# Kernel tuning notes

Measured on AMD Instinct MI355X. Metric: run time of the kernel, lower is better.

Reference implementation:

```python
import math
import jax, jax.numpy as jnp
import numpy as np

B, T, C = 4, 2048, 1024
N_HEAD = 16
HEAD_DIM = C // N_HEAD

def setup_inputs() -> dict:
    key = jax.random.key(0)
    k0, k1, k2, k3, k4 = jax.random.split(key, 5)
    s = 1.0 / math.sqrt(C)
    return {
        "x": jax.random.normal(k0, (B, T, C), dtype=jnp.float32),
        "W_q": jax.random.normal(k1, (C, C), dtype=jnp.float32) * s,
        "W_k": jax.random.normal(k2, (C, C), dtype=jnp.float32) * s,
        "W_v": jax.random.normal(k3, (C, C), dtype=jnp.float32) * s,
        "W_o": jax.random.normal(k4, (C, C), dtype=jnp.float32) * s,
    }

def reference(x, W_q, W_k, W_v, W_o):
    b, t, c = x.shape
    h, hd = N_HEAD, HEAD_DIM
    # nn.Linear(y) = y @ W.T ; project and split heads -> [B, H, T, hd]
    q = (x @ W_q.T).reshape(b, t, h, hd).transpose(0, 2, 1, 3)
    k = (x @ W_k.T).reshape(b, t, h, hd).transpose(0, 2, 1, 3)
    v = (x @ W_v.T).reshape(b, t, h, hd).transpose(0, 2, 1, 3)
    # scores [B, H, T, T], causal mask, stable softmax
    attn = jnp.einsum('bhqd,bhkd->bhqk', q, k) / math.sqrt(hd)
    causal = jnp.tril(jnp.ones((t, t), dtype=bool))
    attn = jnp.where(causal[None, None], attn, -jnp.inf)
    attn = jax.nn.softmax(attn, axis=-1)
    out = jnp.einsum('bhqk,bhkd->bhqd', attn, v)
    out = out.transpose(0, 2, 1, 3).reshape(b, t, c)
    return out @ W_o.T
```

## Files before the change

### kernel.cpp

```cpp
#include <hip/hip_runtime.h>
#include <math.h>

#define Bsz 4
#define Tsz 2048
#define Csz 1024
#define NH  16
#define HD  64

typedef short bf16x8 __attribute__((ext_vector_type(8)));
typedef float f32x4  __attribute__((ext_vector_type(4)));
typedef unsigned short u16;
typedef unsigned int uint;

typedef const __attribute__((address_space(1))) unsigned int gas_uint;
typedef __attribute__((address_space(3))) unsigned int las_uint;

__device__ __forceinline__ void async_cp16(const u16* g, u16* l) {
    __builtin_amdgcn_global_load_lds((gas_uint*)g, (las_uint*)l, 16, 0, 0);
}

__device__ __forceinline__ u16 f2bf(float f) {
    union { float f; unsigned u; } v; v.f = f;
    unsigned r = v.u + 0x7fffu + ((v.u >> 16) & 1u);
    return (u16)(r >> 16);
}

__global__ void cast_kernel(const float* __restrict__ src, u16* __restrict__ dst, int n) {
    int i = (blockIdx.x * blockDim.x + threadIdx.x) * 8;
    if (i + 8 <= n) {
        float4 a = *(const float4*)(src + i);
        float4 b = *(const float4*)(src + i + 4);
        bf16x8 o;
        o[0] = (short)f2bf(a.x); o[1] = (short)f2bf(a.y);
        o[2] = (short)f2bf(a.z); o[3] = (short)f2bf(a.w);
        o[4] = (short)f2bf(b.x); o[5] = (short)f2bf(b.y);
        o[6] = (short)f2bf(b.z); o[7] = (short)f2bf(b.w);
        *(bf16x8*)(dst + i) = o;
    } else {
        for (; i < n; i++) dst[i] = f2bf(src[i]);
    }
}

__global__ void cast3_kernel(const float* __restrict__ s0, const float* __restrict__ s1,
                             const float* __restrict__ s2, u16* __restrict__ dst) {
    const int NW = Csz * Csz;
    int i = (blockIdx.x * blockDim.x + threadIdx.x) * 8;
    int m = i >> 20;
    int local = i & (NW - 1);
    const float* src = (m == 0) ? s0 : (m == 1) ? s1 : s2;
    float4 a = *(const float4*)(src + local);
    float4 b = *(const float4*)(src + local + 4);
    bf16x8 o;
    o[0] = (short)f2bf(a.x); o[1] = (short)f2bf(a.y);
    o[2] = (short)f2bf(a.z); o[3] = (short)f2bf(a.w);
    o[4] = (short)f2bf(b.x); o[5] = (short)f2bf(b.y);
    o[6] = (short)f2bf(b.z); o[7] = (short)f2bf(b.w);
    *(bf16x8*)(dst + i) = o;
}

__global__ void gemm_qkv(const u16* __restrict__ A, const u16* __restrict__ Bm,
                         u16* __restrict__ Qo, u16* __restrict__ Ko, u16* __restrict__ Vo,
                         float qscale) {
    const int K = Csz;
    __shared__ u16 sA[128 * 32];
    __shared__ u16 sB[128 * 32];
    const int tid  = threadIdx.x;
    const int wave = tid >> 6, lane = tid & 63;
    const int lr = lane & 15, lq = lane >> 4;
    const int m0 = blockIdx.y * 128, n0 = blockIdx.x * 128;
    const int wm = (wave & 1) * 64, wn = (wave >> 1) * 64;

    const int srow = lane >> 2;
    const int scol = (lane & 3) * 8;
    const u16* gA = A  + (size_t)(m0 + wave * 32 + srow) * K + scol;
    const u16* gB = Bm + (size_t)(n0 + wave * 32 + srow) * K + scol;
    u16* lA = sA + wave * 1024;
    u16* lB = sB + wave * 1024;

    f32x4 acc[4][4] = {};

    for (int k0 = 0; k0 < K; k0 += 32) {
        __syncthreads();
        async_cp16(gA + k0,                  lA);
        async_cp16(gA + (size_t)16 * K + k0, lA + 512);
        async_cp16(gB + k0,                  lB);
        async_cp16(gB + (size_t)16 * K + k0, lB + 512);
        __syncthreads();

        bf16x8 af[4], bfv[4];
        #pragma unroll
        for (int f = 0; f < 4; f++)
            af[f]  = *(const bf16x8*)(sA + (wm + f * 16 + lr) * 32 + lq * 8);
        #pragma unroll
        for (int f = 0; f < 4; f++)
            bfv[f] = *(const bf16x8*)(sB + (wn + f * 16 + lr) * 32 + lq * 8);
        #pragma unroll
        for (int i = 0; i < 4; i++)
            #pragma unroll
            for (int j = 0; j < 4; j++)
                acc[i][j] = __builtin_amdgcn_mfma_f32_16x16x32_bf16(af[i], bfv[j], acc[i][j], 0, 0, 0);
    }

    const int sel = n0 >> 10;
    const float scale = (sel == 0) ? qscale : 1.0f;
    u16* dst = (sel == 0) ? Qo : (sel == 1) ? Ko : Vo;

    #pragma unroll
    for (int i = 0; i < 4; i++) {
        #pragma unroll
        for (int j = 0; j < 4; j++) {
            #pragma unroll
            for (int r = 0; r < 4; r++) {
                int m = m0 + wm + i * 16 + lq * 4 + r;
                int n = (n0 & 1023) + wn + j * 16 + lr;
                int b = m >> 11, t = m & (Tsz - 1);
                int h = n >> 6,  d = n & (HD - 1);
                u16 bv = f2bf(acc[i][j][r] * scale);
                if (sel == 2)
                    Vo[(((size_t)b * NH + h) * HD + d) * Tsz + t] = bv;
                else
                    dst[(((size_t)b * NH + h) * Tsz + t) * HD + d] = bv;
            }
        }
    }
}

__global__ __launch_bounds__(256, 2)
void gemm_out(const u16* __restrict__ A, const u16* __restrict__ Bm,
              float* __restrict__ out) {
    const int K = Csz, N = Csz;
    __shared__ u16 sA[128 * 32];
    __shared__ u16 sB[128 * 32];
    const int tid  = threadIdx.x;
    const int wave = tid >> 6, lane = tid & 63;
    const int lr = lane & 15, lq = lane >> 4;
    const int m0 = blockIdx.y * 128, n0 = blockIdx.x * 128;
    const int wm = (wave & 1) * 64, wn = (wave >> 1) * 64;

    const int srow = lane >> 2;
    const int scol = (lane & 3) * 8;
    const u16* gA = A  + (size_t)(m0 + wave * 32 + srow) * K + scol;
    const u16* gB = Bm + (size_t)(n0 + wave * 32 + srow) * K + scol;
    u16* lA = sA + wave * 1024;
    u16* lB = sB + wave * 1024;

    f32x4 acc[4][4] = {};

    for (int k0 = 0; k0 < K; k0 += 32) {
        __syncthreads();
        async_cp16(gA + k0,                  lA);
        async_cp16(gA + (size_t)16 * K + k0, lA + 512);
        async_cp16(gB + k0,                  lB);
        async_cp16(gB + (size_t)16 * K + k0, lB + 512);
        __syncthreads();

        bf16x8 af[4], bfv[4];
        #pragma unroll
        for (int f = 0; f < 4; f++)
            af[f]  = *(const bf16x8*)(sA + (wm + f * 16 + lr) * 32 + lq * 8);
        #pragma unroll
        for (int f = 0; f < 4; f++)
            bfv[f] = *(const bf16x8*)(sB + (wn + f * 16 + lr) * 32 + lq * 8);
        #pragma unroll
        for (int i = 0; i < 4; i++)
            #pragma unroll
            for (int j = 0; j < 4; j++)
                acc[i][j] = __builtin_amdgcn_mfma_f32_16x16x32_bf16(af[i], bfv[j], acc[i][j], 0, 0, 0);
    }

    #pragma unroll
    for (int i = 0; i < 4; i++)
        #pragma unroll
        for (int j = 0; j < 4; j++)
            #pragma unroll
            for (int r = 0; r < 4; r++) {
                int m = m0 + wm + i * 16 + lq * 4 + r;
                int n = n0 + wn + j * 16 + lr;
                out[(size_t)m * N + n] = acc[i][j][r];
            }
}

#define LDT 72

__global__ __launch_bounds__(256, 4)
void attn_kernel(const u16* __restrict__ Q, const u16* __restrict__ Kb,
                 const u16* __restrict__ Vt, u16* __restrict__ O) {
    __shared__ u16 sK[64 * LDT];
    __shared__ u16 sV[64 * LDT];
    __shared__ u16 sP[4][16 * LDT];
    const int tid  = threadIdx.x;
    const int wave = tid >> 6, lane = tid & 63;
    const int lr = lane & 15, lq = lane >> 4;
    const int bh = blockIdx.y;
    const int qa = blockIdx.x;
    const int qc = 31 - qa;
    const int ta = qa * 64, tc = qc * 64;

    const u16* Qp = Q  + (size_t)bh * Tsz * HD;
    const u16* Kp = Kb + (size_t)bh * Tsz * HD;
    const u16* Vp = Vt + (size_t)bh * HD * Tsz;

    bf16x8 qfA0 = *(const bf16x8*)(Qp + (size_t)(ta + wave * 16 + lr) * HD + lq * 8);
    bf16x8 qfA1 = *(const bf16x8*)(Qp + (size_t)(ta + wave * 16 + lr) * HD + 32 + lq * 8);
    bf16x8 qfC0 = *(const bf16x8*)(Qp + (size_t)(tc + wave * 16 + lr) * HD + lq * 8);
    bf16x8 qfC1 = *(const bf16x8*)(Qp + (size_t)(tc + wave * 16 + lr) * HD + 32 + lq * 8);

    f32x4 accOA[4] = {}, accOC[4] = {};
    f32x4 accLA = {}, accLC = {};

    bf16x8 ones;
    #pragma unroll
    for (int i = 0; i < 8; i++) ones[i] = (short)0x3F80;

#define PROCESS(T0, QF0, QF1, ACCO, ACCL, DIAG)                                       \
    {                                                                                 \
        f32x4 accS[4];                                                                \
        _Pragma("unroll")                                                             \
        for (int j = 0; j < 4; j++) {                                                 \
            bf16x8 b0 = *(const bf16x8*)(sK + (j * 16 + lr) * LDT + lq * 8);          \
            bf16x8 b1 = *(const bf16x8*)(sK + (j * 16 + lr) * LDT + 32 + lq * 8);     \
            f32x4 z = {};                                                             \
            z = __builtin_amdgcn_mfma_f32_16x16x32_bf16(QF0, b0, z, 0, 0, 0);         \
            z = __builtin_amdgcn_mfma_f32_16x16x32_bf16(QF1, b1, z, 0, 0, 0);         \
            accS[j] = z;                                                              \
        }                                                                             \
        _Pragma("unroll")                                                             \
        for (int r = 0; r < 4; r++) {                                                 \
            const int rowg = (T0) + wave * 16 + lq * 4 + r;                           \
            _Pragma("unroll")                                                         \
            for (int j = 0; j < 4; j++) {                                             \
                float v = accS[j][r];                                                 \
                if (DIAG && (kb * 64 + j * 16 + lr > rowg)) v = -200.0f;              \
                sP[wave][(lq * 4 + r) * LDT + j * 16 + lr] =                          \
                    f2bf(__builtin_amdgcn_exp2f(v));                                  \
            }                                                                         \
        }                                                                             \
        _Pragma("unroll")                                                             \
        for (int ks = 0; ks < 2; ks++) {                                              \
            bf16x8 pf = *(const bf16x8*)(&sP[wave][0] + lr * LDT + ks * 32 + lq * 8); \
            ACCL = __builtin_amdgcn_mfma_f32_16x16x32_bf16(pf, ones, ACCL, 0, 0, 0);  \
            _Pragma("unroll")                                                         \
            for (int j = 0; j < 4; j++) {                                             \
                bf16x8 vf = *(const bf16x8*)(sV + (j * 16 + lr) * LDT + ks * 32 + lq * 8); \
                ACCO[j] = __builtin_amdgcn_mfma_f32_16x16x32_bf16(pf, vf, ACCO[j], 0, 0, 0); \
            }                                                                         \
        }                                                                             \
    }

    for (int kb = 0; kb <= qc; kb++) {
        __syncthreads();
        #pragma unroll
        for (int c = tid; c < 512; c += 256) {
            int row = c >> 3, dc = (c & 7) * 8;
            *(bf16x8*)(sK + row * LDT + dc) =
                *(const bf16x8*)(Kp + (size_t)(kb * 64 + row) * HD + dc);
            *(bf16x8*)(sV + row * LDT + dc) =
                *(const bf16x8*)(Vp + (size_t)row * Tsz + kb * 64 + dc);
        }
        __syncthreads();
        if (kb <= qa) PROCESS(ta, qfA0, qfA1, accOA, accLA, (kb == qa));
        PROCESS(tc, qfC0, qfC1, accOC, accLC, (kb == qc));
    }
#undef PROCESS

    const int b = bh >> 4, h = bh & 15;
    #pragma unroll
    for (int j = 0; j < 4; j++) {
        #pragma unroll
        for (int r = 0; r < 4; r++) {
            int t = wave * 16 + lq * 4 + r;
            int d = j * 16 + lr;
            O[((size_t)b * Tsz + ta + t) * Csz + h * HD + d] = f2bf(accOA[j][r] / accLA[r]);
            O[((size_t)b * Tsz + tc + t) * Csz + h * HD + d] = f2bf(accOC[j][r] / accLC[r]);
        }
    }
}

extern "C" void kernel_launch(void* const* d_in, const int* in_sizes, int n_in,
                              void* d_out, int out_size, void* d_ws, size_t ws_size,
                              hipStream_t stream) {
    const float* x  = (const float*)d_in[0];
    const float* Wq = (const float*)d_in[1];
    const float* Wk = (const float*)d_in[2];
    const float* Wv = (const float*)d_in[3];
    const float* Wo = (const float*)d_in[4];
    float* out = (float*)d_out;

    const size_t NX = (size_t)Bsz * Tsz * Csz;
    const size_t NW = (size_t)Csz * Csz;

    char* ws = (char*)d_ws;
    u16* xb   = (u16*)ws; ws += NX * 2;
    u16* wqkv = (u16*)ws; ws += 3 * NW * 2;
    u16* wob  = (u16*)ws; ws += NW * 2;
    u16* qbuf = (u16*)ws; ws += NX * 2;
    u16* kbuf = (u16*)ws; ws += NX * 2;
    u16* vtb  = (u16*)ws; ws += NX * 2;
    u16* abuf = (u16*)ws; ws += NX * 2;

    cast_kernel<<<dim3((unsigned)(NX / 2048)), 256, 0, stream>>>(x, xb, (int)NX);
    cast3_kernel<<<dim3((unsigned)(3 * NW / 2048)), 256, 0, stream>>>(Wq, Wk, Wv, wqkv);
    cast_kernel<<<dim3((unsigned)(NW / 2048)), 256, 0, stream>>>(Wo, wob, (int)NW);

    const float qscale = 0.125f * 1.44269504088896340736f;
    gemm_qkv<<<dim3(24, 64), 256, 0, stream>>>(xb, wqkv, qbuf, kbuf, vtb, qscale);

    attn_kernel<<<dim3(16, Bsz * NH), 256, 0, stream>>>(qbuf, kbuf, vtb, abuf);

    gemm_out<<<dim3(8, 64), 256, 0, stream>>>(abuf, wob, out);
}
```

Before: 295.4 us.

## Double K-step in GEMMs, vectorize V stores, transpose QK^T to pack P writes

Both GEMM kernels now load two 32-wide K slices per barrier pair, which halves the number of __syncthreads per tile at the cost of double the LDS. The QKV epilogue writes the transposed V tile as packed 4-element bf16 stores. Attention computes S transposed (K as the A operand, Q as B) so each lane holds 4 consecutive keys, allowing packed bf16 stores into the P scratch instead of scalar 16-bit writes. It also uses a cheaper round-half-up bf16 pack, which slightly changes rounding.

```diff
diff --git a/kernel.cpp b/kernel.cpp
--- a/kernel.cpp
+++ b/kernel.cpp
@@ -23,6 +23,11 @@
     union { float f; unsigned u; } v; v.f = f;
     unsigned r = v.u + 0x7fffu + ((v.u >> 16) & 1u);
     return (u16)(r >> 16);
+}
+
+__device__ __forceinline__ uint pkbf(float a, float b) {
+    union { float f; uint u; } x, y; x.f = a; y.f = b;
+    return ((x.u + 0x8000u) >> 16) | ((y.u + 0x8000u) & 0xFFFF0000u);
 }
 
 __global__ void cast_kernel(const float* __restrict__ src, u16* __restrict__ dst, int n) {
@@ -58,12 +63,13 @@
     *(bf16x8*)(dst + i) = o;
 }
 
-__global__ void gemm_qkv(const u16* __restrict__ A, const u16* __restrict__ Bm,
-                         u16* __restrict__ Qo, u16* __restrict__ Ko, u16* __restrict__ Vo,
-                         float qscale) {
+__global__ __launch_bounds__(256, 2)
+void gemm_qkv(const u16* __restrict__ A, const u16* __restrict__ Bm,
+              u16* __restrict__ Qo, u16* __restrict__ Ko, u16* __restrict__ Vo,
+              float qscale) {
     const int K = Csz;
-    __shared__ u16 sA[128 * 32];
-    __shared__ u16 sB[128 * 32];
+    __shared__ u16 sA0[128 * 32], sA1[128 * 32];
+    __shared__ u16 sB0[128 * 32], sB1[128 * 32];
     const int tid  = threadIdx.x;
     const int wave = tid >> 6, lane = tid & 63;
     const int lr = lane & 15, lq = lane >> 4;
@@ -74,54 +80,74 @@
     const int scol = (lane & 3) * 8;
     const u16* gA = A  + (size_t)(m0 + wave * 32 + srow) * K + scol;
     const u16* gB = Bm + (size_t)(n0 + wave * 32 + srow) * K + scol;
-    u16* lA = sA + wave * 1024;
-    u16* lB = sB + wave * 1024;
+    u16* lA0 = sA0 + wave * 1024; u16* lA1 = sA1 + wave * 1024;
+    u16* lB0 = sB0 + wave * 1024; u16* lB1 = sB1 + wave * 1024;
 
     f32x4 acc[4][4] = {};
 
-    for (int k0 = 0; k0 < K; k0 += 32) {
-        __syncthreads();
-        async_cp16(gA + k0,                  lA);
-        async_cp16(gA + (size_t)16 * K + k0, lA + 512);
-        async_cp16(gB + k0,                  lB);
-        async_cp16(gB + (size_t)16 * K + k0, lB + 512);
-        __syncthreads();
-
-        bf16x8 af[4], bfv[4];
-        #pragma unroll
-        for (int f = 0; f < 4; f++)
-            af[f]  = *(const bf16x8*)(sA + (wm + f * 16 + lr) * 32 + lq * 8);
-        #pragma unroll
-        for (int f = 0; f < 4; f++)
-            bfv[f] = *(const bf16x8*)(sB + (wn + f * 16 + lr) * 32 + lq * 8);
+#define QKV_COMPUTE(SA, SB)                                                          \
+    {                                                                                \
+        bf16x8 af[4], bfv[4];                                                        \
+        _Pragma("unroll")                                                            \
+        for (int f = 0; f < 4; f++)                                                  \
+            af[f]  = *(const bf16x8*)((SA) + (wm + f * 16 + lr) * 32 + lq * 8);      \
+        _Pragma("unroll")                                                            \
+        for (int f = 0; f < 4; f++)                                                  \
+            bfv[f] = *(const bf16x8*)((SB) + (wn + f * 16 + lr) * 32 + lq * 8);      \
+        _Pragma("unroll")                                                            \
+        for (int i = 0; i < 4; i++)                                                  \
+            _Pragma("unroll")                                                        \
+            for (int j = 0; j < 4; j++)                                              \
+                acc[i][j] = __builtin_amdgcn_mfma_f32_16x16x32_bf16(af[i], bfv[j], acc[i][j], 0, 0, 0); \
+    }
+
+    for (int k0 = 0; k0 < K; k0 += 64) {
+        __syncthreads();
+        async_cp16(gA + k0,                       lA0);
+        async_cp16(gA + (size_t)16 * K + k0,      lA0 + 512);
+        async_cp16(gA + k0 + 32,                  lA1);
+        async_cp16(gA + (size_t)16 * K + k0 + 32, lA1 + 512);
+        async_cp16(gB + k0,                       lB0);
+        async_cp16(gB + (size_t)16 * K + k0,      lB0 + 512);
+        async_cp16(gB + k0 + 32,                  lB1);
+        async_cp16(gB + (size_t)16 * K + k0 + 32, lB1 + 512);
+        __syncthreads();
+        QKV_COMPUTE(sA0, sB0);
+        QKV_COMPUTE(sA1, sB1);
+    }
+#undef QKV_COMPUTE
+
+    const int sel = n0 >> 10;
+    if (sel == 2) {
+        #pragma unroll
+        for (int i = 0; i < 4; i++) {
+            #pragma unroll
+            for (int j = 0; j < 4; j++) {
+                int m = m0 + wm + i * 16 + lq * 4;
+                int b = m >> 11, t = m & (Tsz - 1);
+                int n = (n0 & 1023) + wn + j * 16 + lr;
+                int h = n >> 6, d = n & (HD - 1);
+                uint2 pk;
+                pk.x = pkbf(acc[i][j][0], acc[i][j][1]);
+                pk.y = pkbf(acc[i][j][2], acc[i][j][3]);
+                *(uint2*)(&Vo[(((size_t)b * NH + h) * HD + d) * Tsz + t]) = pk;
+            }
+        }
+    } else {
+        const float scale = (sel == 0) ? qscale : 1.0f;
+        u16* dst = (sel == 0) ? Qo : Ko;
         #pragma unroll
         for (int i = 0; i < 4; i++)
             #pragma unroll
             for (int j = 0; j < 4; j++)
-                acc[i][j] = __builtin_amdgcn_mfma_f32_16x16x32_bf16(af[i], bfv[j], acc[i][j], 0, 0, 0);
-    }
-
-    const int sel = n0 >> 10;
-    const float scale = (sel == 0) ? qscale : 1.0f;
-    u16* dst = (sel == 0) ? Qo : (sel == 1) ? Ko : Vo;
-
-    #pragma unroll
-    for (int i = 0; i < 4; i++) {
-        #pragma unroll
-        for (int j = 0; j < 4; j++) {
-            #pragma unroll
-            for (int r = 0; r < 4; r++) {
-                int m = m0 + wm + i * 16 + lq * 4 + r;
-                int n = (n0 & 1023) + wn + j * 16 + lr;
-                int b = m >> 11, t = m & (Tsz - 1);
-                int h = n >> 6,  d = n & (HD - 1);
-                u16 bv = f2bf(acc[i][j][r] * scale);
-                if (sel == 2)
-                    Vo[(((size_t)b * NH + h) * HD + d) * Tsz + t] = bv;
-                else
-                    dst[(((size_t)b * NH + h) * Tsz + t) * HD + d] = bv;
-            }
-        }
+                #pragma unroll
+                for (int r = 0; r < 4; r++) {
+                    int m = m0 + wm + i * 16 + lq * 4 + r;
+                    int n = (n0 & 1023) + wn + j * 16 + lr;
+                    int b = m >> 11, t = m & (Tsz - 1);
+                    int h = n >> 6,  d = n & (HD - 1);
+                    dst[(((size_t)b * NH + h) * Tsz + t) * HD + d] = f2bf(acc[i][j][r] * scale);
+                }
     }
 }
 
@@ -129,8 +155,8 @@
 void gemm_out(const u16* __restrict__ A, const u16* __restrict__ Bm,
               float* __restrict__ out) {
     const int K = Csz, N = Csz;
-    __shared__ u16 sA[128 * 32];
-    __shared__ u16 sB[128 * 32];
+    __shared__ u16 sA0[128 * 32], sA1[128 * 32];
+    __shared__ u16 sB0[128 * 32], sB1[128 * 32];
     const int tid  = threadIdx.x;
     const int wave = tid >> 6, lane = tid & 63;
     const int lr = lane & 15, lq = lane >> 4;
@@ -141,32 +167,42 @@
     const int scol = (lane & 3) * 8;
     const u16* gA = A  + (size_t)(m0 + wave * 32 + srow) * K + scol;
     const u16* gB = Bm + (size_t)(n0 + wave * 32 + srow) * K + scol;
-    u16* lA = sA + wave * 1024;
-    u16* lB = sB + wave * 1024;
+    u16* lA0 = sA0 + wave * 1024; u16* lA1 = sA1 + wave * 1024;
+    u16* lB0 = sB0 + wave * 1024; u16* lB1 = sB1 + wave * 1024;
 
     f32x4 acc[4][4] = {};
 
-    for (int k0 = 0; k0 < K; k0 += 32) {
-        __syncthreads();
-        async_cp16(gA + k0,                  lA);
-        async_cp16(gA + (size_t)16 * K + k0, lA + 512);
-        async_cp16(gB + k0,                  lB);
-        async_cp16(gB + (size_t)16 * K + k0, lB + 512);
-        __syncthreads();
-
-        bf16x8 af[4], bfv[4];
-        #pragma unroll
-        for (int f = 0; f < 4; f++)
-            af[f]  = *(const bf16x8*)(sA + (wm + f * 16 + lr) * 32 + lq * 8);
-        #pragma unroll
-        for (int f = 0; f < 4; f++)
-            bfv[f] = *(const bf16x8*)(sB + (wn + f * 16 + lr) * 32 + lq * 8);
-        #pragma unroll
-        for (int i = 0; i < 4; i++)
-            #pragma unroll
-            for (int j = 0; j < 4; j++)
-                acc[i][j] = __builtin_amdgcn_mfma_f32_16x16x32_bf16(af[i], bfv[j], acc[i][j], 0, 0, 0);
-    }
+#define OUT_COMPUTE(SA, SB)                                                          \
+    {                                                                                \
+        bf16x8 af[4], bfv[4];                                                        \
+        _Pragma("unroll")                                                            \
+        for (int f = 0; f < 4; f++)                                                  \
+            af[f]  = *(const bf16x8*)((SA) + (wm + f * 16 + lr) * 32 + lq * 8);      \
+        _Pragma("unroll")                                                            \
+        for (int f = 0; f < 4; f++)                                                  \
+            bfv[f] = *(const bf16x8*)((SB) + (wn + f * 16 + lr) * 32 + lq * 8);      \
+        _Pragma("unroll")                                                            \
+        for (int i = 0; i < 4; i++)                                                  \
+            _Pragma("unroll")                                                        \
+            for (int j = 0; j < 4; j++)                                              \
+                acc[i][j] = __builtin_amdgcn_mfma_f32_16x16x32_bf16(af[i], bfv[j], acc[i][j], 0, 0, 0); \
+    }
+
+    for (int k0 = 0; k0 < K; k0 += 64) {
+        __syncthreads();
+        async_cp16(gA + k0,                       lA0);
+        async_cp16(gA + (size_t)16 * K + k0,      lA0 + 512);
+        async_cp16(gA + k0 + 32,                  lA1);
+        async_cp16(gA + (size_t)16 * K + k0 + 32, lA1 + 512);
+        async_cp16(gB + k0,                       lB0);
+        async_cp16(gB + (size_t)16 * K + k0,      lB0 + 512);
+        async_cp16(gB + k0 + 32,                  lB1);
+        async_cp16(gB + (size_t)16 * K + k0 + 32, lB1 + 512);
+        __syncthreads();
+        OUT_COMPUTE(sA0, sB0);
+        OUT_COMPUTE(sA1, sB1);
+    }
+#undef OUT_COMPUTE
 
     #pragma unroll
     for (int i = 0; i < 4; i++)
@@ -214,26 +250,24 @@
 
 #define PROCESS(T0, QF0, QF1, ACCO, ACCL, DIAG)                                       \
     {                                                                                 \
-        f32x4 accS[4];                                                                \
+        const int qg = (T0) + wave * 16 + lr;                                         \
         _Pragma("unroll")                                                             \
         for (int j = 0; j < 4; j++) {                                                 \
-            bf16x8 b0 = *(const bf16x8*)(sK + (j * 16 + lr) * LDT + lq * 8);          \
-            bf16x8 b1 = *(const bf16x8*)(sK + (j * 16 + lr) * LDT + 32 + lq * 8);     \
+            bf16x8 kf0 = *(const bf16x8*)(sK + (j * 16 + lr) * LDT + lq * 8);         \
+            bf16x8 kf1 = *(const bf16x8*)(sK + (j * 16 + lr) * LDT + 32 + lq * 8);    \
             f32x4 z = {};                                                             \
-            z = __builtin_amdgcn_mfma_f32_16x16x32_bf16(QF0, b0, z, 0, 0, 0);         \
-            z = __builtin_amdgcn_mfma_f32_16x16x32_bf16(QF1, b1, z, 0, 0, 0);         \
-            accS[j] = z;                                                              \
-        }                                                                             \
-        _Pragma("unroll")                                                             \
-        for (int r = 0; r < 4; r++) {                                                 \
-            const int rowg = (T0) + wave * 16 + lq * 4 + r;                           \
-            _Pragma("unroll")                                                         \
-            for (int j = 0; j < 4; j++) {                                             \
-                float v = accS[j][r];                                                 \
-                if (DIAG && (kb * 64 + j * 16 + lr > rowg)) v = -200.0f;              \
-                sP[wave][(lq * 4 + r) * LDT + j * 16 + lr] =                          \
-                    f2bf(__builtin_amdgcn_exp2f(v));                                  \
+            z = __builtin_amdgcn_mfma_f32_16x16x32_bf16(kf0, QF0, z, 0, 0, 0);        \
+            z = __builtin_amdgcn_mfma_f32_16x16x32_bf16(kf1, QF1, z, 0, 0, 0);        \
+            if (DIAG) {                                                               \
+                int kg = kb * 64 + j * 16 + lq * 4;                                   \
+                _Pragma("unroll")                                                     \
+                for (int r = 0; r < 4; r++)                                           \
+                    if (kg + r > qg) z[r] = -200.0f;                                  \
             }                                                                         \
+            uint2 pk2;                                                                \
+            pk2.x = pkbf(__builtin_amdgcn_exp2f(z[0]), __builtin_amdgcn_exp2f(z[1])); \
+            pk2.y = pkbf(__builtin_amdgcn_exp2f(z[2]), __builtin_amdgcn_exp2f(z[3])); \
+            *(uint2*)(&sP[wave][0] + lr * LDT + j * 16 + lq * 4) = pk2;               \
         }                                                                             \
         _Pragma("unroll")                                                             \
         for (int ks = 0; ks < 2; ks++) {                                              \
```

Measured after the change: 322.3 us. 9.1% more time.

## Register-prefetch GEMM tiles and vectorize V transpose stores

Applied to the files above, without the earlier changes.

Replaces the direct global-to-LDS async copies in both projection GEMMs with register prefetch. The next K-slice is loaded into registers while MFMAs run on the current LDS tile, then stored to LDS after the barrier. The transposed V epilogue now packs four consecutive t values into one 8-byte store using round-half-up bf16 conversion, instead of scalar 2-byte stores. This raises register pressure, adds launch bounds to gemm_qkv, and changes V's rounding slightly.

```diff
diff --git a/kernel.cpp b/kernel.cpp
--- a/kernel.cpp
+++ b/kernel.cpp
@@ -12,17 +12,15 @@
 typedef unsigned short u16;
 typedef unsigned int uint;
 
-typedef const __attribute__((address_space(1))) unsigned int gas_uint;
-typedef __attribute__((address_space(3))) unsigned int las_uint;
-
-__device__ __forceinline__ void async_cp16(const u16* g, u16* l) {
-    __builtin_amdgcn_global_load_lds((gas_uint*)g, (las_uint*)l, 16, 0, 0);
-}
-
 __device__ __forceinline__ u16 f2bf(float f) {
     union { float f; unsigned u; } v; v.f = f;
     unsigned r = v.u + 0x7fffu + ((v.u >> 16) & 1u);
     return (u16)(r >> 16);
+}
+
+__device__ __forceinline__ uint pkbf(float a, float b) {
+    union { float f; uint u; } x, y; x.f = a; y.f = b;
+    return ((x.u + 0x8000u) >> 16) | ((y.u + 0x8000u) & 0xFFFF0000u);
 }
 
 __global__ void cast_kernel(const float* __restrict__ src, u16* __restrict__ dst, int n) {
@@ -58,115 +56,96 @@
     *(bf16x8*)(dst + i) = o;
 }
 
-__global__ void gemm_qkv(const u16* __restrict__ A, const u16* __restrict__ Bm,
-                         u16* __restrict__ Qo, u16* __restrict__ Ko, u16* __restrict__ Vo,
-                         float qscale) {
-    const int K = Csz;
-    __shared__ u16 sA[128 * 32];
-    __shared__ u16 sB[128 * 32];
-    const int tid  = threadIdx.x;
-    const int wave = tid >> 6, lane = tid & 63;
-    const int lr = lane & 15, lq = lane >> 4;
-    const int m0 = blockIdx.y * 128, n0 = blockIdx.x * 128;
-    const int wm = (wave & 1) * 64, wn = (wave >> 1) * 64;
-
-    const int srow = lane >> 2;
-    const int scol = (lane & 3) * 8;
-    const u16* gA = A  + (size_t)(m0 + wave * 32 + srow) * K + scol;
-    const u16* gB = Bm + (size_t)(n0 + wave * 32 + srow) * K + scol;
-    u16* lA = sA + wave * 1024;
-    u16* lB = sB + wave * 1024;
-
-    f32x4 acc[4][4] = {};
-
-    for (int k0 = 0; k0 < K; k0 += 32) {
-        __syncthreads();
-        async_cp16(gA + k0,                  lA);
-        async_cp16(gA + (size_t)16 * K + k0, lA + 512);
-        async_cp16(gB + k0,                  lB);
-        async_cp16(gB + (size_t)16 * K + k0, lB + 512);
-        __syncthreads();
-
-        bf16x8 af[4], bfv[4];
-        #pragma unroll
-        for (int f = 0; f < 4; f++)
-            af[f]  = *(const bf16x8*)(sA + (wm + f * 16 + lr) * 32 + lq * 8);
-        #pragma unroll
-        for (int f = 0; f < 4; f++)
-            bfv[f] = *(const bf16x8*)(sB + (wn + f * 16 + lr) * 32 + lq * 8);
+#define GEMM_PIPELINE_BODY(A_, B_, K_)                                               \
+    __shared__ u16 sA[128 * 32];                                                     \
+    __shared__ u16 sB[128 * 32];                                                     \
+    const int tid  = threadIdx.x;                                                    \
+    const int wave = tid >> 6, lane = tid & 63;                                      \
+    const int lr = lane & 15, lq = lane >> 4;                                        \
+    const int m0 = blockIdx.y * 128, n0 = blockIdx.x * 128;                          \
+    const int wm = (wave & 1) * 64, wn = (wave >> 1) * 64;                           \
+    const int srow = lane >> 2;                                                      \
+    const int scol = (lane & 3) * 8;                                                 \
+    const u16* gA = (A_) + (size_t)(m0 + wave * 32 + srow) * (K_) + scol;            \
+    const u16* gB = (B_) + (size_t)(n0 + wave * 32 + srow) * (K_) + scol;            \
+    u16* lA0 = sA + wave * 1024 + srow * 32 + scol;                                  \
+    u16* lA1 = lA0 + 16 * 32;                                                        \
+    u16* lB0 = sB + wave * 1024 + srow * 32 + scol;                                  \
+    u16* lB1 = lB0 + 16 * 32;                                                        \
+    f32x4 acc[4][4] = {};                                                            \
+    bf16x8 pA0 = *(const bf16x8*)(gA);                                               \
+    bf16x8 pA1 = *(const bf16x8*)(gA + (size_t)16 * (K_));                           \
+    bf16x8 pB0 = *(const bf16x8*)(gB);                                               \
+    bf16x8 pB1 = *(const bf16x8*)(gB + (size_t)16 * (K_));                           \
+    for (int k0 = 0; k0 < (K_); k0 += 32) {                                          \
+        __syncthreads();                                                             \
+        *(bf16x8*)lA0 = pA0; *(bf16x8*)lA1 = pA1;                                    \
+        *(bf16x8*)lB0 = pB0; *(bf16x8*)lB1 = pB1;                                    \
+        __syncthreads();                                                             \
+        if (k0 + 32 < (K_)) {                                                        \
+            pA0 = *(const bf16x8*)(gA + k0 + 32);                                    \
+            pA1 = *(const bf16x8*)(gA + (size_t)16 * (K_) + k0 + 32);                \
+            pB0 = *(const bf16x8*)(gB + k0 + 32);                                    \
+            pB1 = *(const bf16x8*)(gB + (size_t)16 * (K_) + k0 + 32);                \
+        }                                                                            \
+        bf16x8 af[4], bfv[4];                                                        \
+        _Pragma("unroll")                                                            \
+        for (int f = 0; f < 4; f++)                                                  \
+            af[f]  = *(const bf16x8*)(sA + (wm + f * 16 + lr) * 32 + lq * 8);        \
+        _Pragma("unroll")                                                            \
+        for (int f = 0; f < 4; f++)                                                  \
+            bfv[f] = *(const bf16x8*)(sB + (wn + f * 16 + lr) * 32 + lq * 8);        \
+        _Pragma("unroll")                                                            \
+        for (int i = 0; i < 4; i++)                                                  \
+            _Pragma("unroll")                                                        \
+            for (int j = 0; j < 4; j++)                                              \
+                acc[i][j] = __builtin_amdgcn_mfma_f32_16x16x32_bf16(af[i], bfv[j], acc[i][j], 0, 0, 0); \
+    }
+
+__global__ __launch_bounds__(256, 2)
+void gemm_qkv(const u16* __restrict__ A, const u16* __restrict__ Bm,
+              u16* __restrict__ Qo, u16* __restrict__ Ko, u16* __restrict__ Vo,
+              float qscale) {
+    GEMM_PIPELINE_BODY(A, Bm, Csz)
+
+    const int sel = n0 >> 10;
+    if (sel == 2) {
+        #pragma unroll
+        for (int i = 0; i < 4; i++) {
+            #pragma unroll
+            for (int j = 0; j < 4; j++) {
+                int m = m0 + wm + i * 16 + lq * 4;
+                int b = m >> 11, t = m & (Tsz - 1);
+                int n = (n0 & 1023) + wn + j * 16 + lr;
+                int h = n >> 6, d = n & (HD - 1);
+                uint2 pk;
+                pk.x = pkbf(acc[i][j][0], acc[i][j][1]);
+                pk.y = pkbf(acc[i][j][2], acc[i][j][3]);
+                *(uint2*)(&Vo[(((size_t)b * NH + h) * HD + d) * Tsz + t]) = pk;
+            }
+        }
+    } else {
+        const float scale = (sel == 0) ? qscale : 1.0f;
+        u16* dst = (sel == 0) ? Qo : Ko;
         #pragma unroll
         for (int i = 0; i < 4; i++)
             #pragma unroll
             for (int j = 0; j < 4; j++)
-                acc[i][j] = __builtin_amdgcn_mfma_f32_16x16x32_bf16(af[i], bfv[j], acc[i][j], 0, 0, 0);
-    }
-
-    const int sel = n0 >> 10;
-    const float scale = (sel == 0) ? qscale : 1.0f;
-    u16* dst = (sel == 0) ? Qo : (sel == 1) ? Ko : Vo;
-
-    #pragma unroll
-    for (int i = 0; i < 4; i++) {
-        #pragma unroll
-        for (int j = 0; j < 4; j++) {
-            #pragma unroll
-            for (int r = 0; r < 4; r++) {
-                int m = m0 + wm + i * 16 + lq * 4 + r;
-                int n = (n0 & 1023) + wn + j * 16 + lr;
-                int b = m >> 11, t = m & (Tsz - 1);
-                int h = n >> 6,  d = n & (HD - 1);
-                u16 bv = f2bf(acc[i][j][r] * scale);
-                if (sel == 2)
-                    Vo[(((size_t)b * NH + h) * HD + d) * Tsz + t] = bv;
-                else
-                    dst[(((size_t)b * NH + h) * Tsz + t) * HD + d] = bv;
-            }
-        }
+                #pragma unroll
+                for (int r = 0; r < 4; r++) {
+                    int m = m0 + wm + i * 16 + lq * 4 + r;
+                    int n = (n0 & 1023) + wn + j * 16 + lr;
+                    int b = m >> 11, t = m & (Tsz - 1);
+                    int h = n >> 6,  d = n & (HD - 1);
+                    dst[(((size_t)b * NH + h) * Tsz + t) * HD + d] = f2bf(acc[i][j][r] * scale);
+                }
     }
 }
 
 __global__ __launch_bounds__(256, 2)
 void gemm_out(const u16* __restrict__ A, const u16* __restrict__ Bm,
               float* __restrict__ out) {
-    const int K = Csz, N = Csz;
-    __shared__ u16 sA[128 * 32];
-    __shared__ u16 sB[128 * 32];
-    const int tid  = threadIdx.x;
-    const int wave = tid >> 6, lane = tid & 63;
-    const int lr = lane & 15, lq = lane >> 4;
-    const int m0 = blockIdx.y * 128, n0 = blockIdx.x * 128;
-    const int wm = (wave & 1) * 64, wn = (wave >> 1) * 64;
-
-    const int srow = lane >> 2;
-    const int scol = (lane & 3) * 8;
-    const u16* gA = A  + (size_t)(m0 + wave * 32 + srow) * K + scol;
-    const u16* gB = Bm + (size_t)(n0 + wave * 32 + srow) * K + scol;
-    u16* lA = sA + wave * 1024;
-    u16* lB = sB + wave * 1024;
-
-    f32x4 acc[4][4] = {};
-
-    for (int k0 = 0; k0 < K; k0 += 32) {
-        __syncthreads();
-        async_cp16(gA + k0,                  lA);
-        async_cp16(gA + (size_t)16 * K + k0, lA + 512);
-        async_cp16(gB + k0,                  lB);
-        async_cp16(gB + (size_t)16 * K + k0, lB + 512);
-        __syncthreads();
-
-        bf16x8 af[4], bfv[4];
-        #pragma unroll
-        for (int f = 0; f < 4; f++)
-            af[f]  = *(const bf16x8*)(sA + (wm + f * 16 + lr) * 32 + lq * 8);
-        #pragma unroll
-        for (int f = 0; f < 4; f++)
-            bfv[f] = *(const bf16x8*)(sB + (wn + f * 16 + lr) * 32 + lq * 8);
-        #pragma unroll
-        for (int i = 0; i < 4; i++)
-            #pragma unroll
-            for (int j = 0; j < 4; j++)
-                acc[i][j] = __builtin_amdgcn_mfma_f32_16x16x32_bf16(af[i], bfv[j], acc[i][j], 0, 0, 0);
-    }
+    GEMM_PIPELINE_BODY(A, Bm, Csz)
 
     #pragma unroll
     for (int i = 0; i < 4; i++)
@@ -176,7 +155,7 @@
             for (int r = 0; r < 4; r++) {
                 int m = m0 + wm + i * 16 + lq * 4 + r;
                 int n = n0 + wn + j * 16 + lr;
-                out[(size_t)m * N + n] = acc[i][j][r];
+                out[(size_t)m * Csz + n] = acc[i][j][r];
             }
 }
 
```

Result: faster. 276.7 us (-6.3%).
